# Kernel optimization log

Measured on AMD Instinct MI355X. Metric: run time of the kernel, lower is better.

Reference implementation:

```python
import jax, jax.numpy as jnp
import numpy as np

H = 2          # h_dim (hard-coded in PPIModel)
L = 4          # n_hid rgcn layers
R = 16         # num_rels
B = 8          # num_bases
N = 1_000_000  # num_nodes
E = 16_000_000 # num_edges


def setup_inputs() -> dict:
    key = jax.random.key(0)
    ks = jax.random.split(key, 10)
    features = jax.random.normal(ks[0], (N * H,), dtype=jnp.float32)
    edge_src = jax.random.randint(ks[1], (E,), 0, N)
    edge_dst = jax.random.randint(ks[2], (E,), 0, N)
    edge_type = jax.random.randint(ks[3], (E,), 0, R)
    norm = jax.random.uniform(ks[4], (E, 1), dtype=jnp.float32)
    # Basis-decomposition params per layer: W_r = sum_b comp[r,b] * V[b]
    V = jax.random.normal(ks[5], (L, B, H, H), dtype=jnp.float32) / np.sqrt(H)
    comp = jax.random.normal(ks[6], (L, R, B), dtype=jnp.float32) / np.sqrt(B)
    bias = jnp.zeros((L, H), dtype=jnp.float32)  # DGL RelGraphConv h_bias (default bias=True)
    w_mlp = jax.random.normal(ks[7], (1, N * H), dtype=jnp.float32) / np.sqrt(N * H)
    b_mlp = jnp.zeros((1,), dtype=jnp.float32)
    return dict(features=features, norm=norm, V=V, comp=comp, bias=bias,
                w_mlp=w_mlp, b_mlp=b_mlp,
                edge_src=edge_src, edge_dst=edge_dst, edge_type=edge_type)


def reference(features, norm, V, comp, bias, w_mlp, b_mlp, edge_src, edge_dst, edge_type):
    x = features.reshape(-1, H)          # [N, 2]
    skip = x
    for i in range(L):
        # relation weights from bases: [R, H, H]
        W = jnp.einsum('rb,bio->rio', comp[i], V[i])
        # message per edge: gather src feats, apply relation weight, scale by norm
        msg = jnp.einsum('ei,eio->eo', x[edge_src], W[edge_type]) * norm  # [E, 2]
        # scatter-sum to destination nodes
        h = jax.ops.segment_sum(msg, edge_dst, num_segments=N) + bias[i]  # [N, 2]
        if i < L - 1:
            h = jax.nn.relu(h)
        x = h
        if i % 2 == 1:
            x = x + skip
            skip = x
    flat = x.reshape(1, N * H)           # [1, 2N]
    logit = flat @ w_mlp.T + b_mlp       # [1, 1]
    return jax.nn.sigmoid(logit)
```

## Files before the change

kernel.cpp:

```cpp
#include <hip/hip_runtime.h>
#include <hip/hip_bf16.h>
#include <hip/hip_fp16.h>

#define HD 2
#define LAYERS 4
#define RELS 16
#define BASES 8

#define NB   512
#define BSH  11
#define SBLK 512
#define TPB  256


__global__ void prep_kernel(const float* __restrict__ V, const float* __restrict__ comp,
                            float* __restrict__ W, float* __restrict__ acc) {
    int idx = threadIdx.x;
    if (idx < LAYERS * RELS * 4) {
        int l  = idx >> 6;
        int r  = (idx >> 2) & (RELS - 1);
        int io = idx & 3;
        float s = 0.f;
        for (int b = 0; b < BASES; ++b)
            s += comp[(l * RELS + r) * BASES + b] * V[(l * BASES + b) * 4 + io];
        W[idx] = s;
    }
    if (idx == 0) *acc = 0.f;
}

__global__ void finalize_kernel(const float* __restrict__ acc,
                                const float* __restrict__ b_mlp,
                                float* __restrict__ out) {
    float v = *acc + b_mlp[0];
    out[0] = 1.f / (1.f + expf(-v));
}


__global__ __launch_bounds__(TPB) void hist_kernel(const int* __restrict__ dst,
                                                   unsigned* __restrict__ blockhist,
                                                   int E, int per) {
    __shared__ unsigned hist[NB];
    for (int i = threadIdx.x; i < NB; i += TPB) hist[i] = 0u;
    __syncthreads();
    int blk = blockIdx.x;
    int e0 = blk * per;
    int e1 = min(e0 + per, E);
    const int4* dst4 = (const int4*)dst;
    int g0 = e0 >> 2, g1 = e1 >> 2;
    for (int g = g0 + threadIdx.x; g < g1; g += TPB) {
        int4 d = dst4[g];
        atomicAdd(&hist[((unsigned)d.x) >> BSH], 1u);
        atomicAdd(&hist[((unsigned)d.y) >> BSH], 1u);
        atomicAdd(&hist[((unsigned)d.z) >> BSH], 1u);
        atomicAdd(&hist[((unsigned)d.w) >> BSH], 1u);
    }
    for (int e = (g1 << 2) + threadIdx.x; e < e1; e += TPB)
        atomicAdd(&hist[((unsigned)dst[e]) >> BSH], 1u);
    __syncthreads();
    for (int i = threadIdx.x; i < NB; i += TPB)
        blockhist[(size_t)blk * NB + i] = hist[i];
}

__global__ __launch_bounds__(TPB) void colscan_kernel(unsigned* __restrict__ blockhist,
                                                      unsigned* __restrict__ totals) {
    int bucket = blockIdx.x;
    int t = threadIdx.x;
    unsigned v0 = blockhist[(size_t)(2 * t)     * NB + bucket];
    unsigned v1 = blockhist[(size_t)(2 * t + 1) * NB + bucket];
    unsigned run = v0 + v1;
    __shared__ unsigned s[TPB];
    s[t] = run;
    __syncthreads();
    for (int off = 1; off < TPB; off <<= 1) {
        unsigned x = (t >= off) ? s[t - off] : 0u;
        __syncthreads();
        s[t] += x;
        __syncthreads();
    }
    unsigned base = s[t] - run;
    blockhist[(size_t)(2 * t)     * NB + bucket] = base;
    blockhist[(size_t)(2 * t + 1) * NB + bucket] = base + v0;
    if (t == TPB - 1) totals[bucket] = s[TPB - 1];
}

__global__ __launch_bounds__(TPB) void scan_kernel(const unsigned* __restrict__ totals,
                                                   unsigned* __restrict__ base) {
    int t = threadIdx.x;
    unsigned v0 = totals[2 * t];
    unsigned v1 = totals[2 * t + 1];
    unsigned run = v0 + v1;
    __shared__ unsigned s[TPB];
    s[t] = run;
    __syncthreads();
    for (int off = 1; off < TPB; off <<= 1) {
        unsigned x = (t >= off) ? s[t - off] : 0u;
        __syncthreads();
        s[t] += x;
        __syncthreads();
    }
    unsigned b0 = s[t] - run;
    base[2 * t]     = b0;
    base[2 * t + 1] = b0 + v0;
    if (t == TPB - 1) base[NB] = s[TPB - 1];
}

__global__ __launch_bounds__(TPB) void scatter_kernel(const int* __restrict__ src,
                                                      const int* __restrict__ dst,
                                                      const int* __restrict__ typ,
                                                      const float* __restrict__ norm,
                                                      const unsigned* __restrict__ blockhist,
                                                      const unsigned* __restrict__ base,
                                                      uint2* __restrict__ packed,
                                                      int E, int per) {
    __shared__ unsigned cnt[NB];
    int blk = blockIdx.x;
    for (int i = threadIdx.x; i < NB; i += TPB)
        cnt[i] = blockhist[(size_t)blk * NB + i] + base[i];
    __syncthreads();
    int e0 = blk * per;
    int e1 = min(e0 + per, E);
    const int4*   src4 = (const int4*)src;
    const int4*   dst4 = (const int4*)dst;
    const int4*   typ4 = (const int4*)typ;
    const float4* nrm4 = (const float4*)norm;
    int g0 = e0 >> 2, g1 = e1 >> 2;

#define PUT(SS, DD, TT, NN)                                                       \
    {                                                                             \
        unsigned _d = (unsigned)(DD);                                             \
        unsigned _bucket = _d >> BSH;                                             \
        unsigned _pos = atomicAdd(&cnt[_bucket], 1u);                             \
        unsigned _w1 = (_d & ((1u << BSH) - 1u)) | (((unsigned)(TT)) << 12) |     \
                       ((unsigned)__half_as_ushort(__float2half_rn(NN)) << 16);   \
        packed[_pos] = make_uint2((unsigned)(SS), _w1);                           \
    }

    for (int g = g0 + threadIdx.x; g < g1; g += TPB) {
        int4 s = src4[g];
        int4 d = dst4[g];
        int4 t = typ4[g];
        float4 nm = nrm4[g];
        PUT(s.x, d.x, t.x, nm.x)
        PUT(s.y, d.y, t.y, nm.y)
        PUT(s.z, d.z, t.z, nm.z)
        PUT(s.w, d.w, t.w, nm.w)
    }
    for (int e = (g1 << 2) + threadIdx.x; e < e1; e += TPB)
        PUT(src[e], dst[e], typ[e], norm[e])
#undef PUT
}

__global__ __launch_bounds__(TPB) void bucket_edge_kernel(
    const uint2* __restrict__ packed,
    const unsigned* __restrict__ base,
    const float2* __restrict__ x2,
    const float* __restrict__ Wl,
    const float* __restrict__ bias2,
    const float2* __restrict__ skip2,
    float2* __restrict__ out2,
    const float2* __restrict__ w2,
    float* __restrict__ acc,
    int N, int do_relu)
{
    __shared__ float acc0[1 << BSH];
    __shared__ float acc1[1 << BSH];
    __shared__ float sW[64];
    __shared__ float wred[4];

    int t = threadIdx.x;
#pragma unroll
    for (int k = 0; k < (1 << BSH) / TPB; ++k) {
        acc0[k * TPB + t] = 0.f;
        acc1[k * TPB + t] = 0.f;
    }
    if (t < 64) sW[t] = Wl[t];
    __syncthreads();

    int b  = blockIdx.x;
    int e0 = (int)base[b];
    int e1 = (int)base[b + 1];

    for (int e = e0 + t; e < e1; e += 2 * TPB) {
        uint2 p0 = packed[e];
        int e2 = e + TPB;
        bool has2 = e2 < e1;
        uint2 p1 = has2 ? packed[e2] : make_uint2(0u, 0u);

        float2 xv0 = x2[p0.x];
        float2 xv1 = has2 ? x2[p1.x] : make_float2(0.f, 0.f);

        {
            unsigned w1  = p0.y;
            unsigned dof = w1 & ((1u << BSH) - 1u);
            int wb = (int)((w1 >> 12) & 15u) << 2;
            float nm = __half2float(__ushort_as_half((unsigned short)(w1 >> 16)));
            float m0 = (xv0.x * sW[wb + 0] + xv0.y * sW[wb + 2]) * nm;
            float m1 = (xv0.x * sW[wb + 1] + xv0.y * sW[wb + 3]) * nm;
            atomicAdd(&acc0[dof], m0);
            atomicAdd(&acc1[dof], m1);
        }
        if (has2) {
            unsigned w1  = p1.y;
            unsigned dof = w1 & ((1u << BSH) - 1u);
            int wb = (int)((w1 >> 12) & 15u) << 2;
            float nm = __half2float(__ushort_as_half((unsigned short)(w1 >> 16)));
            float m0 = (xv1.x * sW[wb + 0] + xv1.y * sW[wb + 2]) * nm;
            float m1 = (xv1.x * sW[wb + 1] + xv1.y * sW[wb + 3]) * nm;
            atomicAdd(&acc0[dof], m0);
            atomicAdd(&acc1[dof], m1);
        }
    }
    __syncthreads();

    float b0 = bias2[0], b1 = bias2[1];
    int nodeBase = b << BSH;
    float part = 0.f;
#pragma unroll
    for (int k = 0; k < (1 << BSH) / TPB; ++k) {
        int i = k * TPB + t;
        int node = nodeBase + i;
        if (node < N) {
            float v0 = acc0[i] + b0;
            float v1 = acc1[i] + b1;
            if (do_relu) { v0 = fmaxf(v0, 0.f); v1 = fmaxf(v1, 0.f); }
            if (skip2) { float2 sv = skip2[node]; v0 += sv.x; v1 += sv.y; }
            if (out2)  out2[node] = make_float2(v0, v1);
            if (w2)    { float2 wv = w2[node]; part += v0 * wv.x + v1 * wv.y; }
        }
    }
    if (w2) {
        for (int off = 32; off > 0; off >>= 1) part += __shfl_down(part, off, 64);
        int lane = t & 63, wv = t >> 6;
        if (lane == 0) wred[wv] = part;
        __syncthreads();
        if (t == 0) atomicAdd(acc, wred[0] + wred[1] + wred[2] + wred[3]);
    }
}


__global__ void zero_kernel(float4* __restrict__ p, int n4) {
    int i = blockIdx.x * blockDim.x + threadIdx.x;
    int stride = gridDim.x * blockDim.x;
    for (; i < n4; i += stride) p[i] = make_float4(0.f, 0.f, 0.f, 0.f);
}

__global__ __launch_bounds__(256) void edge_kernel(
    const float* __restrict__ x, const int* __restrict__ src,
    const int* __restrict__ dst, const int* __restrict__ typ,
    const float* __restrict__ norm, const float* __restrict__ Wl,
    float* __restrict__ h, int E)
{
    __shared__ float sW[64];
    if (threadIdx.x < 64) sW[threadIdx.x] = Wl[threadIdx.x];
    __syncthreads();
    const float2* __restrict__ x2 = (const float2*)x;
    int tid = blockIdx.x * blockDim.x + threadIdx.x;
    int stride = gridDim.x * blockDim.x;
    for (int e = tid; e < E; e += stride) {
        int s = src[e], d = dst[e], t = typ[e];
        float nm = norm[e];
        float2 xv = x2[s];
        int wb = t << 2;
        float m0 = (xv.x * sW[wb + 0] + xv.y * sW[wb + 2]) * nm;
        float m1 = (xv.x * sW[wb + 1] + xv.y * sW[wb + 3]) * nm;
        atomicAdd(&h[2 * (size_t)d],     m0);
        atomicAdd(&h[2 * (size_t)d + 1], m1);
    }
}

__global__ void node_kernel(const float* __restrict__ h, const float* __restrict__ bias_l,
                            const float* __restrict__ skip, float* __restrict__ xout,
                            int N, int do_relu)
{
    float b0 = bias_l[0], b1 = bias_l[1];
    const float2* __restrict__ h2 = (const float2*)h;
    const float2* __restrict__ s2 = (const float2*)skip;
    float2* __restrict__ o2 = (float2*)xout;
    int i = blockIdx.x * blockDim.x + threadIdx.x;
    int stride = gridDim.x * blockDim.x;
    for (; i < N; i += stride) {
        float2 v = h2[i];
        v.x += b0; v.y += b1;
        if (do_relu) { v.x = fmaxf(v.x, 0.f); v.y = fmaxf(v.y, 0.f); }
        if (skip) { float2 sv = s2[i]; v.x += sv.x; v.y += sv.y; }
        o2[i] = v;
    }
}

__global__ __launch_bounds__(256) void dot_kernel(const float* __restrict__ a,
                                                  const float* __restrict__ b,
                                                  float* __restrict__ acc, int n)
{
    int i = blockIdx.x * blockDim.x + threadIdx.x;
    int stride = gridDim.x * blockDim.x;
    float s = 0.f;
    int n4 = n >> 2;
    const float4* __restrict__ a4 = (const float4*)a;
    const float4* __restrict__ b4 = (const float4*)b;
    for (int g = i; g < n4; g += stride) {
        float4 av = a4[g], bv = b4[g];
        s += av.x * bv.x + av.y * bv.y + av.z * bv.z + av.w * bv.w;
    }
    for (int e = (n4 << 2) + i; e < n; e += stride) s += a[e] * b[e];
    for (int off = 32; off > 0; off >>= 1) s += __shfl_down(s, off, 64);
    __shared__ float wsum[4];
    int lane = threadIdx.x & 63, wv = threadIdx.x >> 6;
    if (lane == 0) wsum[wv] = s;
    __syncthreads();
    if (threadIdx.x == 0) atomicAdd(acc, wsum[0] + wsum[1] + wsum[2] + wsum[3]);
}


static inline size_t align256(size_t x) { return (x + 255) & ~(size_t)255; }

extern "C" void kernel_launch(void* const* d_in, const int* in_sizes, int n_in,
                              void* d_out, int out_size, void* d_ws, size_t ws_size,
                              hipStream_t stream) {
    const float* features = (const float*)d_in[0];
    const float* norm     = (const float*)d_in[1];
    const float* V        = (const float*)d_in[2];
    const float* comp     = (const float*)d_in[3];
    const float* bias     = (const float*)d_in[4];
    const float* w_mlp    = (const float*)d_in[5];
    const float* b_mlp    = (const float*)d_in[6];
    const int*   esrc     = (const int*)d_in[7];
    const int*   edst     = (const int*)d_in[8];
    const int*   etyp     = (const int*)d_in[9];

    int NH = in_sizes[0];
    int N  = NH / 2;
    int E  = in_sizes[7];

    char* ws = (char*)d_ws;
    size_t oA    = 0;
    size_t oB    = align256(oA + (size_t)NH * 4);
    size_t oC    = align256(oB + (size_t)NH * 4);
    size_t oW    = align256(oC + (size_t)NH * 4);
    size_t oAcc  = align256(oW + 1024);
    size_t oBase = align256(oAcc + 4);
    size_t oTot  = align256(oBase + (size_t)(NB + 1) * 4);
    size_t oHist = align256(oTot + (size_t)NB * 4);
    size_t oPack = align256(oHist + (size_t)SBLK * NB * 4);
    size_t REQ   = oPack + (size_t)E * 8;

    float* A   = (float*)(ws + oA);
    float* B   = (float*)(ws + oB);
    float* C   = (float*)(ws + oC);
    float* W   = (float*)(ws + oW);
    float* acc = (float*)(ws + oAcc);

    prep_kernel<<<1, 256, 0, stream>>>(V, comp, W, acc);

    if (ws_size >= REQ && N <= (1 << 20)) {
        unsigned* base      = (unsigned*)(ws + oBase);
        unsigned* totals    = (unsigned*)(ws + oTot);
        unsigned* blockhist = (unsigned*)(ws + oHist);
        uint2*    packed    = (uint2*)(ws + oPack);

        int per = (((E + SBLK - 1) / SBLK) + 3) & ~3;

        hist_kernel   <<<SBLK, TPB, 0, stream>>>(edst, blockhist, E, per);
        colscan_kernel<<<NB,   TPB, 0, stream>>>(blockhist, totals);
        scan_kernel   <<<1,    TPB, 0, stream>>>(totals, base);
        scatter_kernel<<<SBLK, TPB, 0, stream>>>(esrc, edst, etyp, norm,
                                                 blockhist, base, packed, E, per);

        int nbkt = (N + (1 << BSH) - 1) >> BSH;
        const float2* feat2 = (const float2*)features;
        const float2* w2    = (const float2*)w_mlp;

        bucket_edge_kernel<<<nbkt, TPB, 0, stream>>>(packed, base, feat2, W + 0,
            bias + 0, nullptr, (float2*)A, nullptr, acc, N, 1);
        bucket_edge_kernel<<<nbkt, TPB, 0, stream>>>(packed, base, (const float2*)A, W + 64,
            bias + 2, feat2, (float2*)B, nullptr, acc, N, 1);
        bucket_edge_kernel<<<nbkt, TPB, 0, stream>>>(packed, base, (const float2*)B, W + 128,
            bias + 4, nullptr, (float2*)C, nullptr, acc, N, 1);
        bucket_edge_kernel<<<nbkt, TPB, 0, stream>>>(packed, base, (const float2*)C, W + 192,
            bias + 6, (const float2*)B, nullptr, w2, acc, N, 0);
    } else {
        int zb = (NH / 4 + 255) / 256;
        int eb = (E / 4 + 255) / 256;
        int nb = (N + 255) / 256;
        int db = (NH / 4 + 255) / 256;

        zero_kernel<<<zb, 256, 0, stream>>>((float4*)A, NH / 4);
        edge_kernel<<<eb, 256, 0, stream>>>(features, esrc, edst, etyp, norm, W + 0, A, E);
        node_kernel<<<nb, 256, 0, stream>>>(A, bias + 0, nullptr, A, N, 1);

        zero_kernel<<<zb, 256, 0, stream>>>((float4*)B, NH / 4);
        edge_kernel<<<eb, 256, 0, stream>>>(A, esrc, edst, etyp, norm, W + 64, B, E);
        node_kernel<<<nb, 256, 0, stream>>>(B, bias + 2, features, B, N, 1);

        zero_kernel<<<zb, 256, 0, stream>>>((float4*)C, NH / 4);
        edge_kernel<<<eb, 256, 0, stream>>>(B, esrc, edst, etyp, norm, W + 128, C, E);
        node_kernel<<<nb, 256, 0, stream>>>(C, bias + 4, nullptr, C, N, 1);

        zero_kernel<<<zb, 256, 0, stream>>>((float4*)A, NH / 4);
        edge_kernel<<<eb, 256, 0, stream>>>(C, esrc, edst, etyp, norm, W + 192, A, E);
        node_kernel<<<nb, 256, 0, stream>>>(A, bias + 6, B, A, N, 0);

        dot_kernel<<<db, 256, 0, stream>>>(A, w_mlp, acc, NH);
    }

    finalize_kernel<<<1, 1, 0, stream>>>(acc, b_mlp, (float*)d_out);
}
```

Measured before the change: 1.128 ms.

## Split each destination bucket across multiple blocks with global atomic merge

Each destination-node bucket's edge range is divided among four blocks, each accumulating in shared memory and then atomically adding into a global H buffer. Bias, relu, skip and the final dot product move into a separate grid-stride epilogue kernel that also re-zeros H. The aim is to raise occupancy beyond roughly one block per bucket, at the cost of global atomics, an extra pass over node features per layer and additional launches.

```diff
diff --git a/kernel.cpp b/kernel.cpp
--- a/kernel.cpp
+++ b/kernel.cpp
@@ -11,6 +11,7 @@
 #define BSH  11
 #define SBLK 512
 #define TPB  256
+#define SPLIT 4
 
 
 __global__ void prep_kernel(const float* __restrict__ V, const float* __restrict__ comp,
@@ -150,22 +151,17 @@
 #undef PUT
 }
 
-__global__ __launch_bounds__(TPB) void bucket_edge_kernel(
+__global__ __launch_bounds__(TPB) void edge_split_kernel(
     const uint2* __restrict__ packed,
     const unsigned* __restrict__ base,
     const float2* __restrict__ x2,
     const float* __restrict__ Wl,
-    const float* __restrict__ bias2,
-    const float2* __restrict__ skip2,
-    float2* __restrict__ out2,
-    const float2* __restrict__ w2,
-    float* __restrict__ acc,
-    int N, int do_relu)
+    float* __restrict__ H,
+    int N)
 {
     __shared__ float acc0[1 << BSH];
     __shared__ float acc1[1 << BSH];
     __shared__ float sW[64];
-    __shared__ float wred[4];
 
     int t = threadIdx.x;
 #pragma unroll
@@ -176,14 +172,19 @@
     if (t < 64) sW[t] = Wl[t];
     __syncthreads();
 
-    int b  = blockIdx.x;
+    int b  = blockIdx.x >> 2;
+    int sl = blockIdx.x & (SPLIT - 1);
     int e0 = (int)base[b];
     int e1 = (int)base[b + 1];
-
-    for (int e = e0 + t; e < e1; e += 2 * TPB) {
+    int len = e1 - e0;
+    int q = len / SPLIT, r = len - q * SPLIT;
+    int s0 = e0 + sl * q + min(sl, r);
+    int s1 = s0 + q + (sl < r ? 1 : 0);
+
+    for (int e = s0 + t; e < s1; e += 2 * TPB) {
         uint2 p0 = packed[e];
         int e2 = e + TPB;
-        bool has2 = e2 < e1;
+        bool has2 = e2 < s1;
         uint2 p1 = has2 ? packed[e2] : make_uint2(0u, 0u);
 
         float2 xv0 = x2[p0.x];
@@ -212,28 +213,47 @@
     }
     __syncthreads();
 
+    size_t fbase = ((size_t)b << BSH) * 2;
+    int fmax = min(2 * (N - (b << BSH)), 2 * (1 << BSH));
+#pragma unroll
+    for (int k = 0; k < (2 * (1 << BSH)) / TPB; ++k) {
+        int j = k * TPB + t;
+        if (j < fmax) {
+            float v = (j & 1) ? acc1[j >> 1] : acc0[j >> 1];
+            atomicAdd(&H[fbase + j], v);
+        }
+    }
+}
+
+__global__ __launch_bounds__(TPB) void epilogue_kernel(
+    float2* __restrict__ H2,
+    const float* __restrict__ bias2,
+    const float2* __restrict__ skip2,
+    float2* __restrict__ out2,
+    const float2* __restrict__ w2,
+    float* __restrict__ acc,
+    int N, int do_relu, int zeroH)
+{
+    __shared__ float wred[TPB / 64];
     float b0 = bias2[0], b1 = bias2[1];
-    int nodeBase = b << BSH;
+    int i = blockIdx.x * TPB + threadIdx.x;
+    int stride = gridDim.x * TPB;
     float part = 0.f;
-#pragma unroll
-    for (int k = 0; k < (1 << BSH) / TPB; ++k) {
-        int i = k * TPB + t;
-        int node = nodeBase + i;
-        if (node < N) {
-            float v0 = acc0[i] + b0;
-            float v1 = acc1[i] + b1;
-            if (do_relu) { v0 = fmaxf(v0, 0.f); v1 = fmaxf(v1, 0.f); }
-            if (skip2) { float2 sv = skip2[node]; v0 += sv.x; v1 += sv.y; }
-            if (out2)  out2[node] = make_float2(v0, v1);
-            if (w2)    { float2 wv = w2[node]; part += v0 * wv.x + v1 * wv.y; }
-        }
+    for (; i < N; i += stride) {
+        float2 v = H2[i];
+        v.x += b0; v.y += b1;
+        if (do_relu) { v.x = fmaxf(v.x, 0.f); v.y = fmaxf(v.y, 0.f); }
+        if (skip2) { float2 sv = skip2[i]; v.x += sv.x; v.y += sv.y; }
+        if (out2)  out2[i] = v;
+        if (w2)    { float2 wv = w2[i]; part += v.x * wv.x + v.y * wv.y; }
+        if (zeroH) H2[i] = make_float2(0.f, 0.f);
     }
     if (w2) {
         for (int off = 32; off > 0; off >>= 1) part += __shfl_down(part, off, 64);
-        int lane = t & 63, wv = t >> 6;
+        int lane = threadIdx.x & 63, wv = threadIdx.x >> 6;
         if (lane == 0) wred[wv] = part;
         __syncthreads();
-        if (t == 0) atomicAdd(acc, wred[0] + wred[1] + wred[2] + wred[3]);
+        if (threadIdx.x == 0) atomicAdd(acc, wred[0] + wred[1] + wred[2] + wred[3]);
     }
 }
 
@@ -335,7 +355,8 @@
     size_t oA    = 0;
     size_t oB    = align256(oA + (size_t)NH * 4);
     size_t oC    = align256(oB + (size_t)NH * 4);
-    size_t oW    = align256(oC + (size_t)NH * 4);
+    size_t oH    = align256(oC + (size_t)NH * 4);
+    size_t oW    = align256(oH + (size_t)NH * 4);
     size_t oAcc  = align256(oW + 1024);
     size_t oBase = align256(oAcc + 4);
     size_t oTot  = align256(oBase + (size_t)(NB + 1) * 4);
@@ -343,11 +364,12 @@
     size_t oPack = align256(oHist + (size_t)SBLK * NB * 4);
     size_t REQ   = oPack + (size_t)E * 8;
 
-    float* A   = (float*)(ws + oA);
-    float* B   = (float*)(ws + oB);
-    float* C   = (float*)(ws + oC);
-    float* W   = (float*)(ws + oW);
-    float* acc = (float*)(ws + oAcc);
+    float* A    = (float*)(ws + oA);
+    float* B    = (float*)(ws + oB);
+    float* C    = (float*)(ws + oC);
+    float* Hbuf = (float*)(ws + oH);
+    float* W    = (float*)(ws + oW);
+    float* acc  = (float*)(ws + oAcc);
 
     prep_kernel<<<1, 256, 0, stream>>>(V, comp, W, acc);
 
@@ -365,18 +387,27 @@
         scatter_kernel<<<SBLK, TPB, 0, stream>>>(esrc, edst, etyp, norm,
                                                  blockhist, base, packed, E, per);
 
+        int zb = (NH / 4 + 255) / 256;
+        zero_kernel<<<zb, 256, 0, stream>>>((float4*)Hbuf, NH / 4);
+
         int nbkt = (N + (1 << BSH) - 1) >> BSH;
+        int egrid = nbkt * SPLIT;
+        int nb2 = min((N + TPB - 1) / TPB, 2048);
         const float2* feat2 = (const float2*)features;
         const float2* w2    = (const float2*)w_mlp;
 
-        bucket_edge_kernel<<<nbkt, TPB, 0, stream>>>(packed, base, feat2, W + 0,
-            bias + 0, nullptr, (float2*)A, nullptr, acc, N, 1);
-        bucket_edge_kernel<<<nbkt, TPB, 0, stream>>>(packed, base, (const float2*)A, W + 64,
-            bias + 2, feat2, (float2*)B, nullptr, acc, N, 1);
-        bucket_edge_kernel<<<nbkt, TPB, 0, stream>>>(packed, base, (const float2*)B, W + 128,
-            bias + 4, nullptr, (float2*)C, nullptr, acc, N, 1);
-        bucket_edge_kernel<<<nbkt, TPB, 0, stream>>>(packed, base, (const float2*)C, W + 192,
-            bias + 6, (const float2*)B, nullptr, w2, acc, N, 0);
+        edge_split_kernel<<<egrid, TPB, 0, stream>>>(packed, base, feat2, W + 0, Hbuf, N);
+        epilogue_kernel  <<<nb2,   TPB, 0, stream>>>((float2*)Hbuf, bias + 0,
+            nullptr, (float2*)A, nullptr, acc, N, 1, 1);
+        edge_split_kernel<<<egrid, TPB, 0, stream>>>(packed, base, (const float2*)A, W + 64, Hbuf, N);
+        epilogue_kernel  <<<nb2,   TPB, 0, stream>>>((float2*)Hbuf, bias + 2,
+            feat2, (float2*)B, nullptr, acc, N, 1, 1);
+        edge_split_kernel<<<egrid, TPB, 0, stream>>>(packed, base, (const float2*)B, W + 128, Hbuf, N);
+        epilogue_kernel  <<<nb2,   TPB, 0, stream>>>((float2*)Hbuf, bias + 4,
+            nullptr, (float2*)C, nullptr, acc, N, 1, 1);
+        edge_split_kernel<<<egrid, TPB, 0, stream>>>(packed, base, (const float2*)C, W + 192, Hbuf, N);
+        epilogue_kernel  <<<nb2,   TPB, 0, stream>>>((float2*)Hbuf, bias + 6,
+            (const float2*)B, nullptr, w2, acc, N, 0, 0);
     } else {
         int zb = (NH / 4 + 255) / 256;
         int eb = (E / 4 + 255) / 256;
```

New measurement: 1.168 ms. 3.6% more time.
